# Performance work log

Hardware: AMD Instinct MI355X
Metric: run time of the kernel (lower is better)

Reference implementation:

```python
import jax, jax.numpy as jnp
import numpy as np

B, T, K = 64, 4096, 48  # batch, seq_len, n_tags


def setup_inputs() -> dict:
    key = jax.random.key(0)
    k1, k2, k3 = jax.random.split(key, 3)
    labels = jax.random.randint(k1, (B, T), 0, K)
    y_true = jax.nn.one_hot(labels, K, dtype=jnp.float32)  # one-hot targets, per dense_loss docstring
    y_pred = jax.random.normal(k2, (B, T, K), dtype=jnp.float32)  # emission scores
    trans = jax.random.normal(k3, (K, K), dtype=jnp.float32) * 0.1  # transition matrix (glorot-ish scale)
    return {"y_true": y_true, "y_pred": y_pred, "trans": trans}


def reference(y_true, y_pred, trans):
    # mask: positions where all emission scores > -1e6 (padding marker)
    mask = jnp.all(y_pred > -1e6, axis=2, keepdims=True).astype(y_pred.dtype)  # (B,T,1)
    y_true = y_true * mask
    y_pred = y_pred * mask

    # target_score: per-label emission score + transition score of the true path
    point_score = jnp.einsum('bni,bni->b', y_true, y_pred)
    trans_score = jnp.einsum('bni,ij,bnj->b', y_true[:, :-1], trans, y_true[:, 1:])
    target = point_score + trans_score  # (B,)

    # log_norm_step recurrence (CRF forward algorithm), fused as a single scan
    init = y_pred[:, 0]  # (B,K)
    xs = jnp.swapaxes(y_pred[:, 1:], 0, 1)  # (T-1,B,K)
    ms = jnp.swapaxes(mask[:, 1:], 0, 1)    # (T-1,B,1)

    def step(s, xm):
        x, m = xm
        # logsumexp over previous-tag axis: s (B,K_prev) + trans (K_prev,K_cur)
        new = jax.scipy.special.logsumexp(s[:, :, None] + trans[None, :, :], axis=1) + x
        s = m * new + (1.0 - m) * s
        return s, None

    s_final, _ = jax.lax.scan(step, init, (xs, ms))
    log_norm = jax.scipy.special.logsumexp(s_final, axis=1)  # (B,)

    # dense_loss returns log_norm - target_score (negative log-likelihood per example)
    return log_norm - target
```

## Files before the change

kernel.cpp:

```cpp
#include <hip/hip_runtime.h>

#define BB 64
#define TT 4096
#define KK 48
#define UST 56
#define PST 56
#define WS_LS_OFF 16384
#define WS_U_OFF 32768
#define SEGBYTES 4608
#define SEGELEMS 2304

typedef __bf16 bf16_t;
typedef bf16_t bf16x8 __attribute__((ext_vector_type(8)));
typedef float f32x4 __attribute__((ext_vector_type(4)));
typedef float f32x16 __attribute__((ext_vector_type(16)));

__device__ __forceinline__ float fexp(float x) {
    return __builtin_amdgcn_exp2f(x * 1.4426950408889634f);
}
__device__ __forceinline__ float flog2(float x) { return __builtin_amdgcn_logf(x); }
__device__ __forceinline__ float rdlanef(float v, int l) {
    return __int_as_float(__builtin_amdgcn_readlane(__float_as_int(v), l));
}
__device__ __forceinline__ unsigned int bf16bits(float f) {
    return (unsigned int)__builtin_bit_cast(unsigned short, (bf16_t)f);
}
__device__ __forceinline__ float bf2f(bf16_t h) {
    return __uint_as_float(((unsigned int)__builtin_bit_cast(unsigned short, h)) << 16);
}
__device__ __forceinline__ unsigned int pktrunc(float lo, float hi) {
    return __builtin_amdgcn_perm(__float_as_uint(hi), __float_as_uint(lo), 0x07060302u);
}

__global__ __launch_bounds__(256, 4) void fused_kernel(
    const float* __restrict__ y_true, const float* __restrict__ y_pred,
    const float* __restrict__ trans, float* __restrict__ ws_target,
    int* __restrict__ ws_ls, bf16_t* __restrict__ ws_u, int nseg) {
    const int s = blockIdx.x, b = blockIdx.y;
    const int seglen = TT / nseg;
    const int nch = seglen / 64;
    const int tid = threadIdx.x;
    const int w = tid >> 6;
    const int lane = tid & 63;
    const int q = lane >> 4;
    const int n = lane & 15;
    const int ncol = 16 * w + n;

    __shared__ __align__(16) float4 exf[2][64 * 13];
    __shared__ __align__(16) bf16_t Ubuf[48 * UST + 16];
    __shared__ unsigned long long pbb[2];
    __shared__ int lsb[4];

    bf16x8 afrag[3][2];
    if (w < 3) {
#pragma unroll
        for (int mt = 0; mt < 3; mt++) {
#pragma unroll
            for (int ks = 0; ks < 2; ks++) {
                bf16x8 f;
#pragma unroll
                for (int j = 0; j < 8; j++) {
                    int k = 32 * ks + 8 * q + j;
                    float v = (k < KK) ? fexp(trans[k * KK + 16 * mt + n]) : 0.0f;
                    f[j] = (bf16_t)v;
                }
                afrag[mt][ks] = f;
            }
        }
    }

    {
        uint4* p = (uint4*)Ubuf;
        for (int i = tid; i < (48 * UST + 16) / 8; i += 256) p[i] = make_uint4(0, 0, 0, 0);
    }
    __syncthreads();
    if (tid < KK) Ubuf[tid * UST + tid] = (bf16_t)1.0f;

    const bf16_t* bptr0 = &Ubuf[ncol * UST + 8 * q];
    const bf16_t* bptr1 = &Ubuf[ncol * UST + 32 + 8 * q];
    bf16_t* wp0 = &Ubuf[ncol * UST + 0 + 4 * q];
    bf16_t* wp1 = &Ubuf[ncol * UST + 16 + 4 * q];
    bf16_t* wp2 = &Ubuf[ncol * UST + 32 + 4 * q];

    f32x4 z4 = {0.0f, 0.0f, 0.0f, 0.0f};
    int ls = 0;
    int cnt = 0;
    float sc_acc = 0.0f;

    auto produce = [&](int ch, int buf) {
        const int t0c = s * seglen + ch * 64;
        const size_t rowbase = ((size_t)b * TT + t0c + lane) * KK;
        const float4* yp4 = (const float4*)(y_pred + rowbase);
        const float4* yt4 = (const float4*)(y_true + rowbase);
        float dot = 0.0f, labf = 0.0f, pmin = 1e30f;
        float4* exrow = &exf[buf][lane * 13];
#pragma unroll 4
        for (int g = 0; g < 12; g++) {
            float4 p = yp4[g];
            float4 a = yt4[g];
            dot = fmaf(a.x, p.x, fmaf(a.y, p.y, fmaf(a.z, p.z, fmaf(a.w, p.w, dot))));
            float e0 = (float)(4 * g);
            labf = fmaf(a.x, e0, fmaf(a.y, e0 + 1.0f, fmaf(a.z, e0 + 2.0f, fmaf(a.w, e0 + 3.0f, labf))));
            pmin = fminf(pmin, fminf(fminf(p.x, p.y), fminf(p.z, p.w)));
            exrow[g] = make_float4(fexp(p.x), fexp(p.y), fexp(p.z), fexp(p.w));
        }
        bool mt_ok = pmin > -1e6f;
        unsigned long long bal = __ballot(mt_ok);
        if (lane == 0) pbb[buf] = bal;

        float labB = 0.0f, pmB = 1e30f;
        const bool hasB = (t0c + 64 < TT);
        if (hasB && lane < 12) {
            const size_t bdbase = ((size_t)b * TT + t0c + 64) * KK;
            float4 a = ((const float4*)(y_true + bdbase))[lane];
            float4 p = ((const float4*)(y_pred + bdbase))[lane];
            float e0 = (float)(4 * lane);
            labB = fmaf(a.x, e0, fmaf(a.y, e0 + 1.0f, fmaf(a.z, e0 + 2.0f, a.w * (e0 + 3.0f))));
            pmB = fminf(fminf(p.x, p.y), fminf(p.z, p.w));
        }
#pragma unroll
        for (int off = 1; off < 16; off <<= 1) {
            labB += __shfl_xor(labB, off);
            pmB = fminf(pmB, __shfl_xor(pmB, off));
        }
        int labB_i = (int)(rdlanef(labB, 0) + 0.5f);
        float mB = (hasB && rdlanef(pmB, 0) > -1e6f) ? 1.0f : 0.0f;

        int labt = (int)(labf + 0.5f);
        float mft = mt_ok ? 1.0f : 0.0f;
        int lnx = __shfl(labt, (lane + 1) & 63);
        float mnx = __shfl(mft, (lane + 1) & 63);
        if (lane == 63) { lnx = labB_i; mnx = mB; }
        sc_acc += mft * dot + mft * mnx * trans[labt * KK + lnx];
    };

    if (w == 3) produce(0, 0);
    __syncthreads();

    for (int ch = 0; ch < nch; ch++) {
        const int cur = ch & 1;
        if (w == 3) {
            if (ch + 1 < nch) produce(ch + 1, cur ^ 1);
        } else {
            const unsigned long long mk = pbb[cur];
            const int tt0 = (s == 0 && ch == 0) ? 1 : 0;
            for (int tt = tt0; tt < 64; tt++) {
                if (!((mk >> tt) & 1ull)) continue;

                bf16x8 bf0 = __builtin_bit_cast(bf16x8, *(const uint4*)bptr0);
                bf16x8 bf1 = __builtin_bit_cast(bf16x8, *(const uint4*)bptr1);

                f32x4 acc0 = __builtin_amdgcn_mfma_f32_16x16x32_bf16(afrag[0][0], bf0, z4, 0, 0, 0);
                acc0 = __builtin_amdgcn_mfma_f32_16x16x32_bf16(afrag[0][1], bf1, acc0, 0, 0, 0);
                f32x4 acc1 = __builtin_amdgcn_mfma_f32_16x16x32_bf16(afrag[1][0], bf0, z4, 0, 0, 0);
                acc1 = __builtin_amdgcn_mfma_f32_16x16x32_bf16(afrag[1][1], bf1, acc1, 0, 0, 0);
                f32x4 acc2 = __builtin_amdgcn_mfma_f32_16x16x32_bf16(afrag[2][0], bf0, z4, 0, 0, 0);
                acc2 = __builtin_amdgcn_mfma_f32_16x16x32_bf16(afrag[2][1], bf1, acc2, 0, 0, 0);

                if (++cnt >= 6) {
                    float v00 = rdlanef(acc0[0], 0);
                    int k = (int)(__float_as_uint(v00) >> 23) - 127;
                    float r = __uint_as_float((unsigned int)(127 - k) << 23);
                    ls += k;
                    cnt = 0;
                    float4 ex0 = exf[cur][tt * 13 + q];
                    ex0.x *= r; ex0.y *= r; ex0.z *= r; ex0.w *= r;
                    *(uint2*)wp0 = make_uint2(pktrunc(acc0[0] * ex0.x, acc0[1] * ex0.y),
                                              pktrunc(acc0[2] * ex0.z, acc0[3] * ex0.w));
                    float4 ex1 = exf[cur][tt * 13 + 4 + q];
                    ex1.x *= r; ex1.y *= r; ex1.z *= r; ex1.w *= r;
                    *(uint2*)wp1 = make_uint2(pktrunc(acc1[0] * ex1.x, acc1[1] * ex1.y),
                                              pktrunc(acc1[2] * ex1.z, acc1[3] * ex1.w));
                    float4 ex2 = exf[cur][tt * 13 + 8 + q];
                    ex2.x *= r; ex2.y *= r; ex2.z *= r; ex2.w *= r;
                    *(uint2*)wp2 = make_uint2(pktrunc(acc2[0] * ex2.x, acc2[1] * ex2.y),
                                              pktrunc(acc2[2] * ex2.z, acc2[3] * ex2.w));
                } else {
                    float4 ex0 = exf[cur][tt * 13 + q];
                    *(uint2*)wp0 = make_uint2(pktrunc(acc0[0] * ex0.x, acc0[1] * ex0.y),
                                              pktrunc(acc0[2] * ex0.z, acc0[3] * ex0.w));
                    float4 ex1 = exf[cur][tt * 13 + 4 + q];
                    *(uint2*)wp1 = make_uint2(pktrunc(acc1[0] * ex1.x, acc1[1] * ex1.y),
                                              pktrunc(acc1[2] * ex1.z, acc1[3] * ex1.w));
                    float4 ex2 = exf[cur][tt * 13 + 8 + q];
                    *(uint2*)wp2 = make_uint2(pktrunc(acc2[0] * ex2.x, acc2[1] * ex2.y),
                                              pktrunc(acc2[2] * ex2.z, acc2[3] * ex2.w));
                }
            }
        }
        __syncthreads();
    }

    if (w == 3) {
#pragma unroll
        for (int off = 32; off; off >>= 1) sc_acc += __shfl_xor(sc_acc, off);
        if (lane == 0) ws_target[b * nseg + s] = sc_acc;
    }

    if (w < 3 && lane == 0) lsb[w] = ls;
    __syncthreads();
    if (w < 3 && lane < KK) {
        const int dl = ls - lsb[0];
        bf16_t* Uo = ws_u + (size_t)(b * nseg + s) * SEGELEMS;
        unsigned int wd[8];
#pragma unroll
        for (int j = 0; j < 8; j++) {
            float f0 = ldexpf(bf2f(Ubuf[(16 * w + 2 * j) * UST + lane]), dl);
            float f1 = ldexpf(bf2f(Ubuf[(16 * w + 2 * j + 1) * UST + lane]), dl);
            wd[j] = bf16bits(f0) | (bf16bits(f1) << 16);
        }
        *(uint4*)(Uo + (size_t)lane * 48 + 16 * w) = make_uint4(wd[0], wd[1], wd[2], wd[3]);
        *(uint4*)(Uo + (size_t)lane * 48 + 16 * w + 8) = make_uint4(wd[4], wd[5], wd[6], wd[7]);
    }
    if (tid == 0) ws_ls[b * nseg + s] = lsb[0];
}

__device__ __forceinline__ int chain_product(const bf16_t* __restrict__ A, bf16_t* Ub, int lane) {
    const int half = lane >> 5;
    const int l31 = lane & 31;
    f32x16 z16;
#pragma unroll
    for (int r = 0; r < 16; r++) z16[r] = 0.0f;

    bf16x8 af[2][3];
#pragma unroll
    for (int mt = 0; mt < 2; mt++) {
        int m = l31 + 32 * mt;
#pragma unroll
        for (int ks = 0; ks < 3; ks++) {
            if (m < KK)
                af[mt][ks] = __builtin_bit_cast(bf16x8, *(const uint4*)&A[(size_t)m * 48 + 16 * ks + 8 * half]);
            else
                af[mt][ks] = __builtin_bit_cast(bf16x8, make_uint4(0, 0, 0, 0));
        }
    }
    bf16x8 bg[3][2];
#pragma unroll
    for (int ks = 0; ks < 3; ks++)
#pragma unroll
        for (int nt = 0; nt < 2; nt++)
            bg[ks][nt] = __builtin_bit_cast(bf16x8, *(const uint4*)&Ub[(l31 + 32 * nt) * PST + 16 * ks + 8 * half]);

    f32x16 acc[4];
#pragma unroll
    for (int mt = 0; mt < 2; mt++)
#pragma unroll
        for (int nt = 0; nt < 2; nt++) {
            f32x16 a0 = __builtin_amdgcn_mfma_f32_32x32x16_bf16(af[mt][0], bg[0][nt], z16, 0, 0, 0);
            a0 = __builtin_amdgcn_mfma_f32_32x32x16_bf16(af[mt][1], bg[1][nt], a0, 0, 0, 0);
            acc[mt * 2 + nt] = __builtin_amdgcn_mfma_f32_32x32x16_bf16(af[mt][2], bg[2][nt], a0, 0, 0, 0);
        }

    float v00 = rdlanef(acc[0][0], 0);
    int k = (int)(__float_as_uint(v00) >> 23) - 127;
    float r = __uint_as_float((unsigned int)(127 - k) << 23);

#pragma unroll
    for (int mt = 0; mt < 2; mt++)
#pragma unroll
        for (int nt = 0; nt < 2; nt++) {
            int c = l31 + 32 * nt;
#pragma unroll
            for (int g = 0; g < 4; g++) {
                int a0 = 32 * mt + 8 * g + 4 * half;
                if (a0 < KK) {
                    const f32x16& Aq = acc[mt * 2 + nt];
                    unsigned int u0 = bf16bits(Aq[4 * g + 0] * r) | (bf16bits(Aq[4 * g + 1] * r) << 16);
                    unsigned int u1 = bf16bits(Aq[4 * g + 2] * r) | (bf16bits(Aq[4 * g + 3] * r) << 16);
                    *(uint2*)&Ub[c * PST + a0] = make_uint2(u0, u1);
                }
            }
        }
    return k;
}

__device__ __forceinline__ int chain_product_ldsA(const bf16_t* As, bf16_t* Ub, int lane) {
    const int half = lane >> 5;
    const int l31 = lane & 31;
    f32x16 z16;
#pragma unroll
    for (int r = 0; r < 16; r++) z16[r] = 0.0f;

    bf16x8 af[2][3];
#pragma unroll
    for (int mt = 0; mt < 2; mt++) {
        int m = l31 + 32 * mt;
#pragma unroll
        for (int ks = 0; ks < 3; ks++) {
            bf16x8 f;
#pragma unroll
            for (int j = 0; j < 8; j++) {
                int k = 16 * ks + 8 * half + j;
                f[j] = (m < KK) ? As[k * PST + m] : (bf16_t)0.0f;
            }
            af[mt][ks] = f;
        }
    }
    bf16x8 bg[3][2];
#pragma unroll
    for (int ks = 0; ks < 3; ks++)
#pragma unroll
        for (int nt = 0; nt < 2; nt++)
            bg[ks][nt] = __builtin_bit_cast(bf16x8, *(const uint4*)&Ub[(l31 + 32 * nt) * PST + 16 * ks + 8 * half]);

    f32x16 acc[4];
#pragma unroll
    for (int mt = 0; mt < 2; mt++)
#pragma unroll
        for (int nt = 0; nt < 2; nt++) {
            f32x16 a0 = __builtin_amdgcn_mfma_f32_32x32x16_bf16(af[mt][0], bg[0][nt], z16, 0, 0, 0);
            a0 = __builtin_amdgcn_mfma_f32_32x32x16_bf16(af[mt][1], bg[1][nt], a0, 0, 0, 0);
            acc[mt * 2 + nt] = __builtin_amdgcn_mfma_f32_32x32x16_bf16(af[mt][2], bg[2][nt], a0, 0, 0, 0);
        }

    float v00 = rdlanef(acc[0][0], 0);
    int k = (int)(__float_as_uint(v00) >> 23) - 127;
    float r = __uint_as_float((unsigned int)(127 - k) << 23);

#pragma unroll
    for (int mt = 0; mt < 2; mt++)
#pragma unroll
        for (int nt = 0; nt < 2; nt++) {
            int c = l31 + 32 * nt;
#pragma unroll
            for (int g = 0; g < 4; g++) {
                int a0 = 32 * mt + 8 * g + 4 * half;
                if (a0 < KK) {
                    const f32x16& Aq = acc[mt * 2 + nt];
                    unsigned int u0 = bf16bits(Aq[4 * g + 0] * r) | (bf16bits(Aq[4 * g + 1] * r) << 16);
                    unsigned int u1 = bf16bits(Aq[4 * g + 2] * r) | (bf16bits(Aq[4 * g + 3] * r) << 16);
                    *(uint2*)&Ub[c * PST + a0] = make_uint2(u0, u1);
                }
            }
        }
    return k;
}

__global__ __launch_bounds__(256) void fold_final_kernel(
    const float* __restrict__ y_pred, const bf16_t* __restrict__ ws_u,
    const int* __restrict__ ws_ls, const float* __restrict__ ws_target,
    float* __restrict__ out, int nseg) {
    const int b = blockIdx.x;
    const int tid = threadIdx.x;
    const int w = tid >> 6, lane = tid & 63;
    const int per = nseg / 4;

    __shared__ __align__(16) bf16_t Ws[4][64 * PST];
    __shared__ int lsp[8];
    if (tid < 8) lsp[tid] = 0;
    __syncthreads();

    {
        const int base = b * nseg + per * w;
        const bf16_t* s0 = ws_u + (size_t)base * SEGELEMS;
        for (int k = 0; k < KK; k++)
            Ws[w][lane * PST + k] = (lane < KK) ? s0[(size_t)k * 48 + lane] : (bf16_t)0.0f;
        int lsk = ws_ls[base];
        for (int j = 1; j < per; j++) {
            lsk += ws_ls[base + j];
            lsk += chain_product(ws_u + (size_t)(base + j) * SEGELEMS, Ws[w], lane);
        }
        if (lane == 0) lsp[w] = lsk;
    }
    __syncthreads();
    int k1 = 0;
    if (w == 0) k1 = chain_product_ldsA(Ws[1], Ws[0], lane);
    if (w == 2) {
        int k2 = chain_product_ldsA(Ws[3], Ws[2], lane);
        if (lane == 0) lsp[5] = k2;
    }
    __syncthreads();

    if (w == 0) {
        int k3 = chain_product_ldsA(Ws[2], Ws[0], lane);
        float L = (float)(lsp[0] + lsp[1] + lsp[2] + lsp[3] + k1 + lsp[5] + k3);

        float x0 = (lane < KK) ? y_pred[(size_t)b * TT * KK + lane] : 0.0f;
        bool ok0 = (lane >= KK) || (x0 > -1e6f);
        bool m0 = (__ballot(ok0) == ~0ull);
        float xeff = (lane < KK) ? (m0 ? x0 : 0.0f) : 0.0f;
        float c0 = rdlanef(xeff, 0);
        float q0 = (lane < KK) ? fexp(xeff - c0) : 0.0f;

        float p = 0.0f;
        if (lane < KK) {
            for (int c = 0; c < KK; c++) {
                float qc = rdlanef(q0, c);
                p = fmaf(bf2f(Ws[0][c * PST + lane]), qc, p);
            }
        }
#pragma unroll
        for (int off = 32; off; off >>= 1) p += __shfl_xor(p, off);

        float tg = (lane < nseg) ? ws_target[b * nseg + lane] : 0.0f;
#pragma unroll
        for (int off = 32; off; off >>= 1) tg += __shfl_xor(tg, off);

        if (lane == 0) {
            out[b] = c0 + 0.6931471805599453f * (L + flog2(p)) - tg;
        }
    }
}

extern "C" void kernel_launch(void* const* d_in, const int* in_sizes, int n_in,
                              void* d_out, int out_size, void* d_ws, size_t ws_size,
                              hipStream_t stream) {
    const float* y_true = (const float*)d_in[0];
    const float* y_pred = (const float*)d_in[1];
    const float* trans = (const float*)d_in[2];
    float* out = (float*)d_out;

    int nseg = 16;
    if (ws_size >= (size_t)WS_U_OFF + (size_t)BB * 32 * SEGBYTES) nseg = 32;

    float* ws_target = (float*)d_ws;
    int* ws_ls = (int*)((char*)d_ws + WS_LS_OFF);
    bf16_t* ws_u = (bf16_t*)((char*)d_ws + WS_U_OFF);

    fused_kernel<<<dim3(nseg, BB), 256, 0, stream>>>(
        y_true, y_pred, trans, ws_target, ws_ls, ws_u, nseg);
    fold_final_kernel<<<BB, 256, 0, stream>>>(y_pred, ws_u, ws_ls, ws_target, out, nseg);
}
```

Baseline: 235.7 us.

## Replace double-buffered producer/consumer pipeline with serialized single-buffer chunk loop

Removes the double-buffered shared-memory staging where warp 3 prefetched and exponentiated the next 64-step chunk while warps 0-2 ran the MFMA recurrence on the current one. Each chunk now loads into a single buffer, with a barrier before the load and another after it. This halves the LDS footprint of the staging buffer, which could raise occupancy or reduce LDS pressure. The cost is that global load latency and exp work are no longer hidden behind the serial recurrence.

Result: no change. 232.8 us (-1.3%).

```diff
diff --git a/kernel.cpp b/kernel.cpp
--- a/kernel.cpp
+++ b/kernel.cpp
@@ -46,9 +46,9 @@
     const int n = lane & 15;
     const int ncol = 16 * w + n;
 
-    __shared__ __align__(16) float4 exf[2][64 * 13];
+    __shared__ __align__(16) float4 exf[64 * 13];
     __shared__ __align__(16) bf16_t Ubuf[48 * UST + 16];
-    __shared__ unsigned long long pbb[2];
+    __shared__ unsigned long long pb;
     __shared__ int lsb[4];
 
     bf16x8 afrag[3][2];
@@ -87,62 +87,57 @@
     int cnt = 0;
     float sc_acc = 0.0f;
 
-    auto produce = [&](int ch, int buf) {
-        const int t0c = s * seglen + ch * 64;
-        const size_t rowbase = ((size_t)b * TT + t0c + lane) * KK;
-        const float4* yp4 = (const float4*)(y_pred + rowbase);
-        const float4* yt4 = (const float4*)(y_true + rowbase);
-        float dot = 0.0f, labf = 0.0f, pmin = 1e30f;
-        float4* exrow = &exf[buf][lane * 13];
+    for (int ch = 0; ch < nch; ch++) {
+        __syncthreads();
+        if (w == 3) {
+            const int t0c = s * seglen + ch * 64;
+            const size_t rowbase = ((size_t)b * TT + t0c + lane) * KK;
+            const float4* yp4 = (const float4*)(y_pred + rowbase);
+            const float4* yt4 = (const float4*)(y_true + rowbase);
+            float dot = 0.0f, labf = 0.0f, pmin = 1e30f;
+            float4* exrow = &exf[lane * 13];
 #pragma unroll 4
-        for (int g = 0; g < 12; g++) {
-            float4 p = yp4[g];
-            float4 a = yt4[g];
-            dot = fmaf(a.x, p.x, fmaf(a.y, p.y, fmaf(a.z, p.z, fmaf(a.w, p.w, dot))));
-            float e0 = (float)(4 * g);
-            labf = fmaf(a.x, e0, fmaf(a.y, e0 + 1.0f, fmaf(a.z, e0 + 2.0f, fmaf(a.w, e0 + 3.0f, labf))));
-            pmin = fminf(pmin, fminf(fminf(p.x, p.y), fminf(p.z, p.w)));
-            exrow[g] = make_float4(fexp(p.x), fexp(p.y), fexp(p.z), fexp(p.w));
-        }
-        bool mt_ok = pmin > -1e6f;
-        unsigned long long bal = __ballot(mt_ok);
-        if (lane == 0) pbb[buf] = bal;
-
-        float labB = 0.0f, pmB = 1e30f;
-        const bool hasB = (t0c + 64 < TT);
-        if (hasB && lane < 12) {
-            const size_t bdbase = ((size_t)b * TT + t0c + 64) * KK;
-            float4 a = ((const float4*)(y_true + bdbase))[lane];
-            float4 p = ((const float4*)(y_pred + bdbase))[lane];
-            float e0 = (float)(4 * lane);
-            labB = fmaf(a.x, e0, fmaf(a.y, e0 + 1.0f, fmaf(a.z, e0 + 2.0f, a.w * (e0 + 3.0f))));
-            pmB = fminf(fminf(p.x, p.y), fminf(p.z, p.w));
-        }
-#pragma unroll
-        for (int off = 1; off < 16; off <<= 1) {
-            labB += __shfl_xor(labB, off);
-            pmB = fminf(pmB, __shfl_xor(pmB, off));
-        }
-        int labB_i = (int)(rdlanef(labB, 0) + 0.5f);
-        float mB = (hasB && rdlanef(pmB, 0) > -1e6f) ? 1.0f : 0.0f;
-
-        int labt = (int)(labf + 0.5f);
-        float mft = mt_ok ? 1.0f : 0.0f;
-        int lnx = __shfl(labt, (lane + 1) & 63);
-        float mnx = __shfl(mft, (lane + 1) & 63);
-        if (lane == 63) { lnx = labB_i; mnx = mB; }
-        sc_acc += mft * dot + mft * mnx * trans[labt * KK + lnx];
-    };
-
-    if (w == 3) produce(0, 0);
-    __syncthreads();
-
-    for (int ch = 0; ch < nch; ch++) {
-        const int cur = ch & 1;
-        if (w == 3) {
-            if (ch + 1 < nch) produce(ch + 1, cur ^ 1);
-        } else {
-            const unsigned long long mk = pbb[cur];
+            for (int g = 0; g < 12; g++) {
+                float4 p = yp4[g];
+                float4 a = yt4[g];
+                dot = fmaf(a.x, p.x, fmaf(a.y, p.y, fmaf(a.z, p.z, fmaf(a.w, p.w, dot))));
+                float e0 = (float)(4 * g);
+                labf = fmaf(a.x, e0, fmaf(a.y, e0 + 1.0f, fmaf(a.z, e0 + 2.0f, fmaf(a.w, e0 + 3.0f, labf))));
+                pmin = fminf(pmin, fminf(fminf(p.x, p.y), fminf(p.z, p.w)));
+                exrow[g] = make_float4(fexp(p.x), fexp(p.y), fexp(p.z), fexp(p.w));
+            }
+            bool mt_ok = pmin > -1e6f;
+            unsigned long long bal = __ballot(mt_ok);
+            if (lane == 0) pb = bal;
+
+            float labB = 0.0f, pmB = 1e30f;
+            const bool hasB = (t0c + 64 < TT);
+            if (hasB && lane < 12) {
+                const size_t bdbase = ((size_t)b * TT + t0c + 64) * KK;
+                float4 a = ((const float4*)(y_true + bdbase))[lane];
+                float4 p = ((const float4*)(y_pred + bdbase))[lane];
+                float e0 = (float)(4 * lane);
+                labB = fmaf(a.x, e0, fmaf(a.y, e0 + 1.0f, fmaf(a.z, e0 + 2.0f, a.w * (e0 + 3.0f))));
+                pmB = fminf(fminf(p.x, p.y), fminf(p.z, p.w));
+            }
+#pragma unroll
+            for (int off = 1; off < 16; off <<= 1) {
+                labB += __shfl_xor(labB, off);
+                pmB = fminf(pmB, __shfl_xor(pmB, off));
+            }
+            int labB_i = (int)(rdlanef(labB, 0) + 0.5f);
+            float mB = (hasB && rdlanef(pmB, 0) > -1e6f) ? 1.0f : 0.0f;
+
+            int labt = (int)(labf + 0.5f);
+            float mft = mt_ok ? 1.0f : 0.0f;
+            int lnx = __shfl(labt, (lane + 1) & 63);
+            float mnx = __shfl(mft, (lane + 1) & 63);
+            if (lane == 63) { lnx = labB_i; mnx = mB; }
+            sc_acc += mft * dot + mft * mnx * trans[labt * KK + lnx];
+        }
+        __syncthreads();
+        if (w < 3) {
+            const unsigned long long mk = pb;
             const int tt0 = (s == 0 && ch == 0) ? 1 : 0;
             for (int tt = tt0; tt < 64; tt++) {
                 if (!((mk >> tt) & 1ull)) continue;
@@ -163,32 +158,31 @@
                     float r = __uint_as_float((unsigned int)(127 - k) << 23);
                     ls += k;
                     cnt = 0;
-                    float4 ex0 = exf[cur][tt * 13 + q];
+                    float4 ex0 = exf[tt * 13 + q];
                     ex0.x *= r; ex0.y *= r; ex0.z *= r; ex0.w *= r;
                     *(uint2*)wp0 = make_uint2(pktrunc(acc0[0] * ex0.x, acc0[1] * ex0.y),
                                               pktrunc(acc0[2] * ex0.z, acc0[3] * ex0.w));
-                    float4 ex1 = exf[cur][tt * 13 + 4 + q];
+                    float4 ex1 = exf[tt * 13 + 4 + q];
                     ex1.x *= r; ex1.y *= r; ex1.z *= r; ex1.w *= r;
                     *(uint2*)wp1 = make_uint2(pktrunc(acc1[0] * ex1.x, acc1[1] * ex1.y),
                                               pktrunc(acc1[2] * ex1.z, acc1[3] * ex1.w));
-                    float4 ex2 = exf[cur][tt * 13 + 8 + q];
+                    float4 ex2 = exf[tt * 13 + 8 + q];
                     ex2.x *= r; ex2.y *= r; ex2.z *= r; ex2.w *= r;
                     *(uint2*)wp2 = make_uint2(pktrunc(acc2[0] * ex2.x, acc2[1] * ex2.y),
                                               pktrunc(acc2[2] * ex2.z, acc2[3] * ex2.w));
                 } else {
-                    float4 ex0 = exf[cur][tt * 13 + q];
+                    float4 ex0 = exf[tt * 13 + q];
                     *(uint2*)wp0 = make_uint2(pktrunc(acc0[0] * ex0.x, acc0[1] * ex0.y),
                                               pktrunc(acc0[2] * ex0.z, acc0[3] * ex0.w));
-                    float4 ex1 = exf[cur][tt * 13 + 4 + q];
+                    float4 ex1 = exf[tt * 13 + 4 + q];
                     *(uint2*)wp1 = make_uint2(pktrunc(acc1[0] * ex1.x, acc1[1] * ex1.y),
                                               pktrunc(acc1[2] * ex1.z, acc1[3] * ex1.w));
-                    float4 ex2 = exf[cur][tt * 13 + 8 + q];
+                    float4 ex2 = exf[tt * 13 + 8 + q];
                     *(uint2*)wp2 = make_uint2(pktrunc(acc2[0] * ex2.x, acc2[1] * ex2.y),
                                               pktrunc(acc2[2] * ex2.z, acc2[3] * ex2.w));
                 }
             }
         }
-        __syncthreads();
     }
 
     if (w == 3) {
```
